# Optimization experiments

Hardware: AMD Instinct MI355X
Metric: run time of the kernel (lower is better)

## Reference

```python
import jax, jax.numpy as jnp
import numpy as np

LN_EPS = 1e-5


def _layernorm(x, g, b):
    m = jnp.mean(x, axis=-1, keepdims=True)
    v = jnp.mean((x - m) ** 2, axis=-1, keepdims=True)
    return (x - m) * jax.lax.rsqrt(v + LN_EPS) * g + b


def _gcn_conv(x, row, col, ew, W, b):
    # linear projection
    x = x @ W + b  # [N, out]
    n = x.shape[0]
    # weighted degree per source node (index_add over row)
    deg = jax.ops.segment_sum(ew, row, num_segments=n)  # [N]
    safe = jnp.where(deg > 0, deg, 1.0)
    dis = jnp.where(deg > 0, jax.lax.rsqrt(safe), 0.0)  # deg^-0.5, inf -> 0
    norm = dis[row] * ew * dis[col]  # [E]
    # gather-scale-scatter aggregation
    return jax.ops.segment_sum(norm[:, None] * x[col], row, num_segments=n)


def setup_inputs() -> dict:
    key = jax.random.key(0)
    ks = jax.random.split(key, 8)
    N, E, D_IN, D_H, D_OUT = 50000, 800000, 384, 256, 128
    x = jax.random.normal(ks[0], (N, D_IN), dtype=jnp.float32)
    edge_index = jax.random.randint(ks[1], (2, E), 0, N, dtype=jnp.int64)
    edge_weight = jax.random.uniform(ks[2], (E,), dtype=jnp.float32)
    W1 = jax.random.normal(ks[3], (D_IN, D_H), dtype=jnp.float32) * 0.02
    b1 = jnp.zeros((D_H,), dtype=jnp.float32)
    W2 = jax.random.normal(ks[4], (D_H, D_OUT), dtype=jnp.float32) * 0.02
    b2 = jnp.zeros((D_OUT,), dtype=jnp.float32)
    g1 = jnp.ones((D_H,), dtype=jnp.float32)
    be1 = jnp.zeros((D_H,), dtype=jnp.float32)
    g2 = jnp.ones((D_OUT,), dtype=jnp.float32)
    be2 = jnp.zeros((D_OUT,), dtype=jnp.float32)
    return {"x": x, "edge_index": edge_index, "edge_weight": edge_weight,
            "W1": W1, "b1": b1, "W2": W2, "b2": b2,
            "g1": g1, "be1": be1, "g2": g2, "be2": be2}


def reference(x, edge_index, edge_weight, W1, b1, W2, b2, g1, be1, g2, be2):
    row, col = edge_index[0], edge_index[1]
    h = _gcn_conv(x, row, col, edge_weight, W1, b1)
    h = _layernorm(h, g1, be1)
    h = jax.nn.relu(h)
    # dropout is identity in eval mode
    h = _gcn_conv(h, row, col, edge_weight, W2, b2)
    h = _layernorm(h, g2, be2)
    return h
```

## Files before the change

kernel.cpp:

```cpp
#include <hip/hip_runtime.h>


constexpr float LN_EPS = 1e-5f;
constexpr int   SLOTS  = 64;

typedef __attribute__((ext_vector_type(8))) short short8;
typedef __attribute__((ext_vector_type(4))) float f32x4;
typedef __attribute__((ext_vector_type(2))) float f32x2;

static __device__ __forceinline__ unsigned short f2bf(float f) {
    unsigned u = __float_as_uint(f);
    u += 0x7FFFu + ((u >> 16) & 1u);
    return (unsigned short)(u >> 16);
}
static __device__ __forceinline__ float bf2f(unsigned short h) {
    return __uint_as_float(((unsigned)h) << 16);
}
static __device__ __forceinline__ short8 f2bf8(float4 a, float4 b) {
    short8 r;
    r[0] = (short)f2bf(a.x); r[1] = (short)f2bf(a.y);
    r[2] = (short)f2bf(a.z); r[3] = (short)f2bf(a.w);
    r[4] = (short)f2bf(b.x); r[5] = (short)f2bf(b.y);
    r[6] = (short)f2bf(b.z); r[7] = (short)f2bf(b.w);
    return r;
}

#if defined(__has_builtin)
#if __has_builtin(__builtin_amdgcn_global_load_lds)
#define HAS_GLL 1
#endif
#endif

#ifdef HAS_GLL
static __device__ __forceinline__ void gll16(const void* g, void* l) {
    __builtin_amdgcn_global_load_lds(
        (__attribute__((address_space(1))) void*)g,
        (__attribute__((address_space(3))) void*)l, 16, 0, 0);
}
#endif

static __device__ __forceinline__ int swz(int r) {
    return (r & 3) ^ ((r >> 2) & 3);
}

__global__ __launch_bounds__(256) void k_pre(
    const int* __restrict__ row, const int* __restrict__ col,
    const float* __restrict__ ew, int* __restrict__ cnt,
    unsigned* __restrict__ edges4, int E, int histBlocks,
    const float* __restrict__ W1, const float* __restrict__ W2,
    const float* __restrict__ x,
    unsigned short* __restrict__ W1P, unsigned short* __restrict__ W2P,
    unsigned short* __restrict__ xb, int nwin)
{
    constexpr int K1 = 384, N1 = 256, K2 = 256, N2 = 128;
    constexpr int WTB = (K1 * N1 + K2 * N2) / 256;
    const int bx = blockIdx.x;
    if (bx < histBlocks) {
        int e = bx * 256 + threadIdx.x;
        if (e >= E) return;
        int r = row[e];
        int o = atomicAdd(cnt + r, 1);
        if (o < SLOTS)
            edges4[(size_t)r * SLOTS + o] =
                ((unsigned)col[e] << 16) | (unsigned)f2bf(ew[e]);
    } else if (bx < histBlocks + WTB) {
        int o = (bx - histBlocks) * 256 + threadIdx.x;
        if (o < K1 * N1) {
            int cc = o & 31, n = (o >> 5) % N1, p = o / (N1 * 32);
            int c = cc >> 3, j = cc & 7;
            int k = p * 32 + (((c ^ swz(n & 15)) & 3) << 3) + j;
            W1P[o] = f2bf(W1[(size_t)k * N1 + n]);
        } else {
            int o2 = o - K1 * N1;
            int cc = o2 & 31, n = (o2 >> 5) % N2, p = o2 / (N2 * 32);
            int c = cc >> 3, j = cc & 7;
            int k = p * 32 + (((c ^ swz(n & 15)) & 3) << 3) + j;
            W2P[o2] = f2bf(W2[(size_t)k * N2 + n]);
        }
    } else {
        int w = (bx - histBlocks - WTB) * 256 + threadIdx.x;
        if (w >= nwin) return;
        int r = w / 12, win = w - r * 12;
        int s = swz(r & 15);
        const float* src = x + (size_t)r * 384 + win * 32;
        unsigned short* dst = xb + (size_t)r * 384 + win * 32;
        #pragma unroll
        for (int c = 0; c < 4; ++c) {
            int cs = c ^ s;
            float4 a = *(const float4*)(src + cs * 8);
            float4 b = *(const float4*)(src + cs * 8 + 4);
            *(short8*)(dst + c * 8) = f2bf8(a, b);
        }
    }
}

__global__ __launch_bounds__(256) void k_dis(
    const int* __restrict__ cnt, const unsigned* __restrict__ edges4,
    float* __restrict__ dis, int n)
{
    const int gw   = (blockIdx.x * 256 + threadIdx.x) >> 6;
    const int lane = threadIdx.x & 63;
    if (gw >= n) return;
    int c = cnt[gw]; if (c > SLOTS) c = SLOTS;
    float v = 0.0f;
    if (lane < c)
        v = bf2f((unsigned short)(edges4[(size_t)gw * SLOTS + lane] & 0xffffu));
    #pragma unroll
    for (int off = 32; off; off >>= 1) v += __shfl_xor(v, off);
    if (lane == 0) dis[gw] = v > 0.0f ? rsqrtf(v) : 0.0f;
}

template<int NFULL, int K>
__global__ __launch_bounds__(256, 4) void k_gemm_mfma(
    const unsigned short* __restrict__ A, const unsigned short* __restrict__ BP,
    const float* __restrict__ bias, unsigned short* __restrict__ C, int M)
{
    constexpr int BM = 64, BN = 128, BK = 32;
    constexpr int MR = 4, NF = 2;
    constexpr int AB = BM * BK * 2;
    constexpr int BB = BN * BK * 2;
    constexpr int TB = AB + BB;

    __shared__ char smem[2 * TB];

    const int t    = threadIdx.x;
    const int lane = t & 63;
    const int wid  = t >> 6;
    const int row0 = blockIdx.x * BM;
    const int col0 = blockIdx.y * BN;
    const int fr   = lane & 15;
    const int fq   = lane >> 4;
    const int nbw  = wid * 32;
    const int nt   = K / BK;

    const int cOff = ((fq ^ swz(fr)) & 3) << 3;

    f32x4 acc[MR][NF] = {};

    auto srcA = [&](int slot, int k0) -> const void* {
        int ra = slot >> 2, ca = slot & 3;
        int gr = row0 + ra; if (gr >= M) gr = M - 1;
        return (const void*)(A + (size_t)gr * K + k0 + ca * 8);
    };
    auto srcB = [&](int slot, int st) -> const void* {
        int rb = slot >> 2, cb = slot & 3;
        return (const void*)(BP + ((size_t)st * NFULL + col0 + rb) * 32 + cb * 8);
    };

    auto compute = [&](char* buf) {
        const unsigned short* As = (const unsigned short*)buf;
        const unsigned short* Bs = (const unsigned short*)(buf + AB);
        short8 af[MR], bfr[NF];
        #pragma unroll
        for (int i = 0; i < MR; ++i)
            af[i] = *(const short8*)(As + (i * 16 + fr) * 32 + cOff);
        #pragma unroll
        for (int j = 0; j < NF; ++j)
            bfr[j] = *(const short8*)(Bs + (nbw + j * 16 + fr) * 32 + cOff);
        #pragma unroll
        for (int i = 0; i < MR; ++i)
            #pragma unroll
            for (int j = 0; j < NF; ++j)
                acc[i][j] = __builtin_amdgcn_mfma_f32_16x16x32_bf16(
                    af[i], bfr[j], acc[i][j], 0, 0, 0);
    };

#ifdef HAS_GLL
    auto stage = [&](int buf, int st) {
        char* As = smem + buf * TB;
        char* Bs = As + AB;
        gll16(srcA(t, st * BK), As + t * 16);
        gll16(srcB(t, st), Bs + t * 16);
        gll16(srcB(256 + t, st), Bs + (256 + t) * 16);
    };

    stage(0, 0);
    __syncthreads();
    int cur = 0;
    for (int st = 0; st < nt; ++st) {
        if (st + 1 < nt) stage(cur ^ 1, st + 1);
        compute(smem + cur * TB);
        __syncthreads();
        cur ^= 1;
    }
#else
    for (int st = 0; st < nt; ++st) {
        int4 ar = *(const int4*)srcA(t, st * BK);
        int4 b0 = *(const int4*)srcB(t, st);
        int4 b1 = *(const int4*)srcB(256 + t, st);
        __syncthreads();
        *(int4*)(smem + t * 16) = ar;
        *(int4*)(smem + AB + t * 16) = b0;
        *(int4*)(smem + AB + (256 + t) * 16) = b1;
        __syncthreads();
        compute(smem);
    }
#endif

    #pragma unroll
    for (int i = 0; i < MR; ++i) {
        #pragma unroll
        for (int j = 0; j < NF; ++j) {
            const int c = col0 + nbw + j * 16 + fr;
            const float bvv = bias[c];
            #pragma unroll
            for (int r = 0; r < 4; ++r) {
                const int rr = row0 + i * 16 + fq * 4 + r;
                if (rr < M)
                    C[(size_t)rr * NFULL + c] = f2bf(acc[i][j][r] + bvv);
            }
        }
    }
}

template<int D, bool RELU, bool OUTBF, bool SWZ>
__global__ __launch_bounds__(256) void k_agg_ln(
    const unsigned short* __restrict__ feat, const int* __restrict__ cnt,
    const unsigned* __restrict__ edges4, const float* __restrict__ dis,
    const float* __restrict__ g, const float* __restrict__ b,
    void* __restrict__ outv, int n)
{
    constexpr int EV  = 16;
    constexpr int LPR = D / EV;
    constexpr int EPI = 64 / LPR;
    const int gw   = (blockIdx.x * 256 + threadIdx.x) >> 6;
    const int lane = threadIdx.x & 63;
    if (gw >= n) return;

    const int sub = lane / LPR;
    const int el  = (lane % LPR) * EV;

    int j1 = cnt[gw]; if (j1 > SLOTS) j1 = SLOTS;
    const unsigned* eb = edges4 + (size_t)gw * SLOTS;
    const float disr = dis[gw];

    f32x2 acc[8] = {};

    unsigned e0 = (sub < j1)       ? eb[sub]       : 0u;
    unsigned e1 = (EPI + sub < j1) ? eb[EPI + sub] : 0u;
    float dc0 = dis[e0 >> 16];
    uint4 u0, u1;
    {
        const unsigned short* p = feat + (size_t)(e0 >> 16) * D + el;
        u0 = *(const uint4*)p;
        u1 = *(const uint4*)(p + 8);
    }

    for (int j = 0; j < j1; j += EPI) {
        unsigned e2 = (j + 2 * EPI + sub < j1) ? eb[j + 2 * EPI + sub] : 0u;
        float dc1 = dis[e1 >> 16];
        const unsigned short* p = feat + (size_t)(e1 >> 16) * D + el;
        uint4 v0 = *(const uint4*)p;
        uint4 v1 = *(const uint4*)(p + 8);

        const float wv = bf2f((unsigned short)(e0 & 0xffffu)) * dc0;
        const unsigned a[8] = {u0.x, u0.y, u0.z, u0.w, u1.x, u1.y, u1.z, u1.w};
        #pragma unroll
        for (int i = 0; i < 8; ++i) {
            f32x2 h;
            h.x = __uint_as_float(a[i] << 16);
            h.y = __uint_as_float(a[i] & 0xffff0000u);
            acc[i] += h * wv;
        }
        u0 = v0; u1 = v1; e0 = e1; e1 = e2; dc0 = dc1;
    }

    #pragma unroll
    for (int off = LPR; off < 64; off <<= 1)
        #pragma unroll
        for (int i = 0; i < 8; ++i) {
            acc[i].x += __shfl_xor(acc[i].x, off);
            acc[i].y += __shfl_xor(acc[i].y, off);
        }

    #pragma unroll
    for (int i = 0; i < 8; ++i) acc[i] *= disr;

    float s = 0.0f;
    #pragma unroll
    for (int i = 0; i < 8; ++i) s += acc[i].x + acc[i].y;
    #pragma unroll
    for (int off = 32; off; off >>= 1) s += __shfl_xor(s, off);
    const float m = s * (1.0f / (EPI * D));

    float q = 0.0f;
    #pragma unroll
    for (int i = 0; i < 8; ++i) {
        float dx = acc[i].x - m, dy = acc[i].y - m;
        q += dx * dx + dy * dy;
    }
    #pragma unroll
    for (int off = 32; off; off >>= 1) q += __shfl_xor(q, off);
    const float r = rsqrtf(q * (1.0f / (EPI * D)) + LN_EPS);

    if (lane < LPR) {
        float o[16];
        #pragma unroll
        for (int i = 0; i < 4; ++i) {
            float4 gv = *(const float4*)(g + el + i * 4);
            float4 bv = *(const float4*)(b + el + i * 4);
            const float vals[4] = {acc[2 * i].x, acc[2 * i].y,
                                   acc[2 * i + 1].x, acc[2 * i + 1].y};
            const float gg[4] = {gv.x, gv.y, gv.z, gv.w};
            const float bb[4] = {bv.x, bv.y, bv.z, bv.w};
            #pragma unroll
            for (int k2 = 0; k2 < 4; ++k2) {
                float tv = (vals[k2] - m) * r * gg[k2] + bb[k2];
                if constexpr (RELU) tv = fmaxf(tv, 0.0f);
                o[i * 4 + k2] = tv;
            }
        }
        if constexpr (OUTBF) {
            short8 lo, hi;
            #pragma unroll
            for (int i = 0; i < 8; ++i) {
                lo[i] = (short)f2bf(o[i]);
                hi[i] = (short)f2bf(o[8 + i]);
            }
            unsigned short* ob = (unsigned short*)outv + (size_t)gw * D;
            const int w0 = el & ~31;
            const int c0 = (el >> 3) & 3;
            const int sA = SWZ ? swz(gw & 15) : 0;
            *(short8*)(ob + w0 + (((c0 ^ sA) & 3) << 3))       = lo;
            *(short8*)(ob + w0 + ((((c0 + 1) ^ sA) & 3) << 3)) = hi;
        } else {
            float* op = (float*)outv + (size_t)gw * D + el;
            *(float4*)(op)      = make_float4(o[0],  o[1],  o[2],  o[3]);
            *(float4*)(op + 4)  = make_float4(o[4],  o[5],  o[6],  o[7]);
            *(float4*)(op + 8)  = make_float4(o[8],  o[9],  o[10], o[11]);
            *(float4*)(op + 12) = make_float4(o[12], o[13], o[14], o[15]);
        }
    }
}

extern "C" void kernel_launch(void* const* d_in, const int* in_sizes, int n_in,
                              void* d_out, int out_size, void* d_ws, size_t ws_size,
                              hipStream_t stream)
{
    (void)n_in; (void)out_size; (void)ws_size;

    constexpr int DIN = 384, DH = 256, DOUT = 128;

    const float* x   = (const float*)d_in[0];
    const int*   ei  = (const int*)  d_in[1];
    const float* ew  = (const float*)d_in[2];
    const float* W1  = (const float*)d_in[3];
    const float* b1  = (const float*)d_in[4];
    const float* W2  = (const float*)d_in[5];
    const float* b2  = (const float*)d_in[6];
    const float* g1  = (const float*)d_in[7];
    const float* be1 = (const float*)d_in[8];
    const float* g2  = (const float*)d_in[9];
    const float* be2 = (const float*)d_in[10];
    float* out = (float*)d_out;

    const int N = in_sizes[0] / DIN;
    const int E = in_sizes[2];
    const int* row = ei;
    const int* col = ei + E;

    char* w = (char*)d_ws;
    auto carve = [&](size_t bytes) {
        char* p = w;
        w += (bytes + 255) & ~(size_t)255;
        return p;
    };
    int*            cnt    = (int*)     carve((size_t)N * 4);
    float*          dis    = (float*)   carve((size_t)N * 4);
    unsigned*       edges4 = (unsigned*)carve((size_t)N * SLOTS * 4);
    unsigned short* W1P    = (unsigned short*)carve((size_t)DIN * DH * 2);
    unsigned short* W2P    = (unsigned short*)carve((size_t)DH * DOUT * 2);
    unsigned short* x_bf   = (unsigned short*)carve((size_t)N * DIN * 2);
    unsigned short* h1     = (unsigned short*)carve((size_t)N * DH * 2);
    unsigned short* h1ln   = (unsigned short*)carve((size_t)N * DH * 2);
    unsigned short* h2     = (unsigned short*)carve((size_t)N * DOUT * 2);

    const int gE = (E + 255) / 256;
    const int gW = (N + 3) / 4;
    const int gG = (N + 63) / 64;
    const int gX = (N * 12 + 255) / 256;
    constexpr int WTB = (DIN * DH + DH * DOUT) / 256;

    hipMemsetAsync(cnt, 0, (size_t)N * 4, stream);
    k_pre<<<gE + WTB + gX, 256, 0, stream>>>(
        row, col, ew, cnt, edges4, E, gE, W1, W2, x, W1P, W2P, x_bf, N * 12);
    k_dis<<<gW, 256, 0, stream>>>(cnt, edges4, dis, N);

    {
        dim3 grid(gG, DH / 128);
        k_gemm_mfma<DH, DIN><<<grid, 256, 0, stream>>>(x_bf, W1P, b1, h1, N);
    }
    k_agg_ln<DH, true, true, true><<<gW, 256, 0, stream>>>(
        h1, cnt, edges4, dis, g1, be1, h1ln, N);

    {
        dim3 grid(gG, DOUT / 128);
        k_gemm_mfma<DOUT, DH><<<grid, 256, 0, stream>>>(h1ln, W2P, b2, h2, N);
    }
    k_agg_ln<DOUT, false, false, false><<<gW, 256, 0, stream>>>(
        h2, cnt, edges4, dis, g2, be2, out, N);
}
```

Measured before the change: 219.4 us.

## Fuse fp32-to-bf16 conversion of x into first GEMM A-tile load

Removes the separate x-to-bf16 conversion pass from the pre-kernel. The first GEMM now reads fp32 x directly, converts it to bf16 in registers with the swizzle applied, and stores it to LDS while B tiles still use the async global-to-LDS loads. The pre-kernel also interleaves histogram and weight-packing blocks. This saves a full write and re-read of the bf16 copy of x. In exchange, the GEMM grid (two column blocks) now reads fp32 x twice, converts it twice, and adds an extra barrier per k-step.

New measurement: 212.3 us. 1.03x faster.

```diff
diff --git a/kernel.cpp b/kernel.cpp
--- a/kernel.cpp
+++ b/kernel.cpp
@@ -48,23 +48,31 @@
     const float* __restrict__ ew, int* __restrict__ cnt,
     unsigned* __restrict__ edges4, int E, int histBlocks,
     const float* __restrict__ W1, const float* __restrict__ W2,
-    const float* __restrict__ x,
-    unsigned short* __restrict__ W1P, unsigned short* __restrict__ W2P,
-    unsigned short* __restrict__ xb, int nwin)
+    unsigned short* __restrict__ W1P, unsigned short* __restrict__ W2P)
 {
     constexpr int K1 = 384, N1 = 256, K2 = 256, N2 = 128;
     constexpr int WTB = (K1 * N1 + K2 * N2) / 256;
+
     const int bx = blockIdx.x;
-    if (bx < histBlocks) {
-        int e = bx * 256 + threadIdx.x;
+    const int m2 = 2 * (histBlocks < WTB ? histBlocks : WTB);
+    bool isHist;
+    int  id;
+    if (bx < m2) { isHist = !(bx & 1); id = bx >> 1; }
+    else {
+        id = (m2 >> 1) + (bx - m2);
+        isHist = histBlocks > WTB;
+    }
+
+    if (isHist) {
+        int e = id * 256 + threadIdx.x;
         if (e >= E) return;
         int r = row[e];
         int o = atomicAdd(cnt + r, 1);
         if (o < SLOTS)
             edges4[(size_t)r * SLOTS + o] =
                 ((unsigned)col[e] << 16) | (unsigned)f2bf(ew[e]);
-    } else if (bx < histBlocks + WTB) {
-        int o = (bx - histBlocks) * 256 + threadIdx.x;
+    } else {
+        int o = id * 256 + threadIdx.x;
         if (o < K1 * N1) {
             int cc = o & 31, n = (o >> 5) % N1, p = o / (N1 * 32);
             int c = cc >> 3, j = cc & 7;
@@ -77,20 +85,6 @@
             int k = p * 32 + (((c ^ swz(n & 15)) & 3) << 3) + j;
             W2P[o2] = f2bf(W2[(size_t)k * N2 + n]);
         }
-    } else {
-        int w = (bx - histBlocks - WTB) * 256 + threadIdx.x;
-        if (w >= nwin) return;
-        int r = w / 12, win = w - r * 12;
-        int s = swz(r & 15);
-        const float* src = x + (size_t)r * 384 + win * 32;
-        unsigned short* dst = xb + (size_t)r * 384 + win * 32;
-        #pragma unroll
-        for (int c = 0; c < 4; ++c) {
-            int cs = c ^ s;
-            float4 a = *(const float4*)(src + cs * 8);
-            float4 b = *(const float4*)(src + cs * 8 + 4);
-            *(short8*)(dst + c * 8) = f2bf8(a, b);
-        }
     }
 }
 
@@ -110,9 +104,9 @@
     if (lane == 0) dis[gw] = v > 0.0f ? rsqrtf(v) : 0.0f;
 }
 
-template<int NFULL, int K>
+template<bool AF32, int NFULL, int K>
 __global__ __launch_bounds__(256, 4) void k_gemm_mfma(
-    const unsigned short* __restrict__ A, const unsigned short* __restrict__ BP,
+    const void* __restrict__ Av, const unsigned short* __restrict__ BP,
     const float* __restrict__ bias, unsigned short* __restrict__ C, int M)
 {
     constexpr int BM = 64, BN = 128, BK = 32;
@@ -135,16 +129,26 @@
 
     const int cOff = ((fq ^ swz(fr)) & 3) << 3;
 
+    const float*          Af = (const float*)Av;
+    const unsigned short* Ab = (const unsigned short*)Av;
+
     f32x4 acc[MR][NF] = {};
 
     auto srcA = [&](int slot, int k0) -> const void* {
         int ra = slot >> 2, ca = slot & 3;
         int gr = row0 + ra; if (gr >= M) gr = M - 1;
-        return (const void*)(A + (size_t)gr * K + k0 + ca * 8);
+        return (const void*)(Ab + (size_t)gr * K + k0 + ca * 8);
     };
     auto srcB = [&](int slot, int st) -> const void* {
         int rb = slot >> 2, cb = slot & 3;
         return (const void*)(BP + ((size_t)st * NFULL + col0 + rb) * 32 + cb * 8);
+    };
+    auto ldA32 = [&](int st, short8& rv) {
+        int ra = t >> 2, ca = t & 3;
+        int cs = ca ^ (swz(ra & 15) & 3);
+        int gr = row0 + ra; if (gr >= M) gr = M - 1;
+        const float* p = Af + (size_t)gr * K + st * BK + cs * 8;
+        rv = f2bf8(*(const float4*)p, *(const float4*)(p + 4));
     };
 
     auto compute = [&](char* buf) {
@@ -166,30 +170,56 @@
     };
 
 #ifdef HAS_GLL
-    auto stage = [&](int buf, int st) {
-        char* As = smem + buf * TB;
-        char* Bs = As + AB;
-        gll16(srcA(t, st * BK), As + t * 16);
-        gll16(srcB(t, st), Bs + t * 16);
-        gll16(srcB(256 + t, st), Bs + (256 + t) * 16);
-    };
-
-    stage(0, 0);
-    __syncthreads();
-    int cur = 0;
-    for (int st = 0; st < nt; ++st) {
-        if (st + 1 < nt) stage(cur ^ 1, st + 1);
-        compute(smem + cur * TB);
+    if constexpr (AF32) {
+        auto gllB = [&](int buf, int st) {
+            char* Bs = smem + buf * TB + AB;
+            gll16(srcB(t, st), Bs + t * 16);
+            gll16(srcB(256 + t, st), Bs + (256 + t) * 16);
+        };
+        short8 a0;
+        ldA32(0, a0);
+        gllB(0, 0);
         __syncthreads();
-        cur ^= 1;
+        *(short8*)(smem + t * 16) = a0;
+        __syncthreads();
+        int cur = 0;
+        for (int st = 0; st < nt; ++st) {
+            short8 an;
+            if (st + 1 < nt) { ldA32(st + 1, an); gllB(cur ^ 1, st + 1); }
+            compute(smem + cur * TB);
+            __syncthreads();
+            if (st + 1 < nt)
+                *(short8*)(smem + (cur ^ 1) * TB + t * 16) = an;
+            __syncthreads();
+            cur ^= 1;
+        }
+    } else {
+        auto stage = [&](int buf, int st) {
+            char* As = smem + buf * TB;
+            char* Bs = As + AB;
+            gll16(srcA(t, st * BK), As + t * 16);
+            gll16(srcB(t, st), Bs + t * 16);
+            gll16(srcB(256 + t, st), Bs + (256 + t) * 16);
+        };
+        stage(0, 0);
+        __syncthreads();
+        int cur = 0;
+        for (int st = 0; st < nt; ++st) {
+            if (st + 1 < nt) stage(cur ^ 1, st + 1);
+            compute(smem + cur * TB);
+            __syncthreads();
+            cur ^= 1;
+        }
     }
 #else
     for (int st = 0; st < nt; ++st) {
-        int4 ar = *(const int4*)srcA(t, st * BK);
+        short8 ar;
+        if constexpr (AF32) ldA32(st, ar);
+        else                ar = *(const short8*)srcA(t, st * BK);
         int4 b0 = *(const int4*)srcB(t, st);
         int4 b1 = *(const int4*)srcB(256 + t, st);
         __syncthreads();
-        *(int4*)(smem + t * 16) = ar;
+        *(short8*)(smem + t * 16) = ar;
         *(int4*)(smem + AB + t * 16) = b0;
         *(int4*)(smem + AB + (256 + t) * 16) = b1;
         __syncthreads();
@@ -370,7 +400,6 @@
     unsigned*       edges4 = (unsigned*)carve((size_t)N * SLOTS * 4);
     unsigned short* W1P    = (unsigned short*)carve((size_t)DIN * DH * 2);
     unsigned short* W2P    = (unsigned short*)carve((size_t)DH * DOUT * 2);
-    unsigned short* x_bf   = (unsigned short*)carve((size_t)N * DIN * 2);
     unsigned short* h1     = (unsigned short*)carve((size_t)N * DH * 2);
     unsigned short* h1ln   = (unsigned short*)carve((size_t)N * DH * 2);
     unsigned short* h2     = (unsigned short*)carve((size_t)N * DOUT * 2);
@@ -378,24 +407,23 @@
     const int gE = (E + 255) / 256;
     const int gW = (N + 3) / 4;
     const int gG = (N + 63) / 64;
-    const int gX = (N * 12 + 255) / 256;
     constexpr int WTB = (DIN * DH + DH * DOUT) / 256;
 
     hipMemsetAsync(cnt, 0, (size_t)N * 4, stream);
-    k_pre<<<gE + WTB + gX, 256, 0, stream>>>(
-        row, col, ew, cnt, edges4, E, gE, W1, W2, x, W1P, W2P, x_bf, N * 12);
+    k_pre<<<gE + WTB, 256, 0, stream>>>(
+        row, col, ew, cnt, edges4, E, gE, W1, W2, W1P, W2P);
     k_dis<<<gW, 256, 0, stream>>>(cnt, edges4, dis, N);
 
     {
         dim3 grid(gG, DH / 128);
-        k_gemm_mfma<DH, DIN><<<grid, 256, 0, stream>>>(x_bf, W1P, b1, h1, N);
+        k_gemm_mfma<true, DH, DIN><<<grid, 256, 0, stream>>>(x, W1P, b1, h1, N);
     }
     k_agg_ln<DH, true, true, true><<<gW, 256, 0, stream>>>(
         h1, cnt, edges4, dis, g1, be1, h1ln, N);
 
     {
         dim3 grid(gG, DOUT / 128);
-        k_gemm_mfma<DOUT, DH><<<grid, 256, 0, stream>>>(h1ln, W2P, b2, h2, N);
+        k_gemm_mfma<false, DOUT, DH><<<grid, 256, 0, stream>>>(h1ln, W2P, b2, h2, N);
     }
     k_agg_ln<DOUT, false, false, false><<<gW, 256, 0, stream>>>(
         h2, cnt, edges4, dis, g2, be2, out, N);
```
